# Performance work log

Measured on AMD Instinct MI355X. Metric: run time of the kernel, lower is better.

The kernel has to match this reference:

```python
import jax, jax.numpy as jnp
import numpy as np
import math

# Config (matches init_kwargs / input_specs)
N_ENT = 50000      # number of entities
N_REL = 500        # number of relations
HID = 64           # args.hidden_dim = per-axis dim d; entity dim = 3d, relation dim = 4d
E = 500000         # number of edges
EMB_RANGE = 1.0    # embedding_range
PI = 3.1415926235897933


def setup_inputs() -> dict:
    key = jax.random.key(0)
    k1, k2, k3, k4, k5 = jax.random.split(key, 5)
    entities = jax.random.normal(k1, (N_ENT, 3 * HID), dtype=jnp.float32)
    relations = jax.random.normal(k2, (N_REL, 4 * HID), dtype=jnp.float32)
    head = jax.random.randint(k3, (E,), 0, N_ENT, dtype=jnp.int32)
    rel = jax.random.randint(k4, (E,), 0, N_REL, dtype=jnp.int32)
    tail = jax.random.randint(k5, (E,), 0, N_ENT, dtype=jnp.int32)
    edge_index = jnp.stack([head, rel, tail], axis=0)  # (3, E)
    return {"entities": entities, "relations": relations, "edge_index": edge_index}


def do_trans(ent, rel):
    """Rot3DE rotation: rotate 3D entity point (per feature dim) by the
    quaternion encoded in rel = (axis_x, axis_y, axis_z, theta). is_head_rel=True branch.
    ent: (E, 3d), rel: (E, 4d) -> (E, 4d)"""
    ex, ey, ez = jnp.split(ent, 3, axis=-1)            # each (E, d)
    rx, ry, rz, theta = jnp.split(rel, 4, axis=-1)     # each (E, d)
    theta = theta / (EMB_RANGE / PI)
    sin = jnp.sin(theta)
    w = jnp.cos(theta)
    # F.normalize(stack([sin*rx, sin*ry, sin*rz]), dim=0): unit rotation axis (sign of sin folded in)
    t = jnp.stack([sin * rx, sin * ry, sin * rz], axis=0)  # (3, E, d)
    norm = jnp.sqrt(jnp.sum(t * t, axis=0, keepdims=True))
    n = t / jnp.maximum(norm, 1e-12)
    # quaternion q = (w, u) with u = |sin(theta)| * unit_axis  (sin sign already in n)
    s = jnp.sqrt(jnp.clip(1.0 - w * w, 0.0, None))
    ux, uy, uz = s * n[0], s * n[1], s * n[2]
    # Hamilton product q (x) p with pure quaternion p = (0, ex, ey, ez)  [head direction]
    x_score = w * ex + (uy * ez - uz * ey)
    y_score = w * ey + (uz * ex - ux * ez)
    z_score = w * ez + (ux * ey - uy * ex)
    w_score = -(ux * ex + uy * ey + uz * ez)
    return jnp.concatenate([x_score, y_score, z_score, w_score], axis=-1)  # (E, 4d)


def reference(entities, relations, edge_index):
    head, rel_id, tail = edge_index[0], edge_index[1], edge_index[2]
    # eff_do_trans's unique-based dedup is a pure compute optimization; the
    # math is identical to the direct per-edge transform below.
    qv = do_trans(entities[head], relations[rel_id])  # (E, 4d) keys/values
    # GAT_update: key = [gathered tail entity (3d) ; zeros(d)]
    k = jnp.concatenate(
        [entities[tail], jnp.zeros((E, HID), dtype=entities.dtype)], axis=-1
    )  # (E, 4d)
    embed_dim = 4 * HID
    alpha = jnp.sum(k * qv, axis=-1) / math.sqrt(embed_dim)  # (E,)
    # scatter_softmax over destination nodes (stable segment softmax)
    m = jax.ops.segment_max(alpha, tail, num_segments=N_ENT)
    m = jnp.where(jnp.isfinite(m), m, 0.0)  # empty segments
    e = jnp.exp(alpha - m[tail])
    denom = jax.ops.segment_sum(e, tail, num_segments=N_ENT)
    attn = e / denom[tail]  # (E,)
    # weighted scatter_add -> (N_ENT, 4d)
    out = jax.ops.segment_sum(qv * attn[:, None], tail, num_segments=N_ENT)
    return out
```

## Files before the change

### kernel.cpp

```cpp
#include <hip/hip_runtime.h>
#include <stdint.h>
#include <math.h>

#define HID 64
#define PI_F 3.14159262235897933f

__device__ __forceinline__ unsigned short f2bf(float f) {
    unsigned u = __float_as_uint(f);
    return (unsigned short)((u + 0x7FFFu + ((u >> 16) & 1u)) >> 16);
}
__device__ __forceinline__ float bflo(unsigned v) { return __uint_as_float(v << 16); }
__device__ __forceinline__ float bfhi(unsigned v) { return __uint_as_float(v & 0xFFFF0000u); }

__global__ void prep(const float* __restrict__ rel, uint2* __restrict__ quat16, int nrel,
                     const int* __restrict__ eidx, int E, int* __restrict__ hist,
                     const float* __restrict__ ent, uint4* __restrict__ ent16, int nconv,
                     int qblocks, int eblocks) {
    const int b = blockIdx.x;
    if (b < qblocks) {
        int i = b * 256 + threadIdx.x;
        if (i >= nrel * HID) return;
        int r = i >> 6, j = i & 63;
        const float* base = rel + (size_t)r * 4 * HID;
        float rx = base[j];
        float ry = base[HID + j];
        float rz = base[2 * HID + j];
        float th = base[3 * HID + j];
        float theta = th * PI_F;
        float sn = sinf(theta);
        float w  = cosf(theta);
        float tx = sn * rx, ty = sn * ry, tz = sn * rz;
        float norm = sqrtf(tx * tx + ty * ty + tz * tz);
        float inv = 1.0f / fmaxf(norm, 1e-12f);
        float s = sqrtf(fmaxf(1.0f - w * w, 0.0f));
        float ux = s * tx * inv, uy = s * ty * inv, uz = s * tz * inv;
        quat16[i] = make_uint2(((unsigned)f2bf(ux) << 16) | f2bf(w),
                               ((unsigned)f2bf(uz) << 16) | f2bf(uy));
    } else if (b < qblocks + eblocks) {
        int e = (b - qblocks) * 256 + threadIdx.x;
        if (e >= E) return;
        atomicAdd(hist + eidx[2 * E + e], 1);
    } else {
        int u = (b - qblocks - eblocks) * 256 + threadIdx.x;
        if (u >= nconv) return;
        const float4* src = (const float4*)ent + 2 * (size_t)u;
        float4 a = src[0], c = src[1];
        ent16[u] = make_uint4(((unsigned)f2bf(a.y) << 16) | f2bf(a.x),
                              ((unsigned)f2bf(a.w) << 16) | f2bf(a.z),
                              ((unsigned)f2bf(c.y) << 16) | f2bf(c.x),
                              ((unsigned)f2bf(c.w) << 16) | f2bf(c.z));
    }
}

__global__ void scan1(const int* __restrict__ hist, int* __restrict__ base,
                      int* __restrict__ partial, int n) {
    __shared__ int buf[256];
    int tid = threadIdx.x;
    int gid = blockIdx.x * 256 + tid;
    int v = (gid < n) ? hist[gid] : 0;
    buf[tid] = v;
    __syncthreads();
    #pragma unroll
    for (int off = 1; off < 256; off <<= 1) {
        int x = (tid >= off) ? buf[tid - off] : 0;
        __syncthreads();
        buf[tid] += x;
        __syncthreads();
    }
    if (gid < n) base[gid] = buf[tid] - v;
    if (tid == 255) partial[blockIdx.x] = buf[255];
}

__global__ void scan23(int* __restrict__ base, int* __restrict__ base2,
                       const int* __restrict__ partial,
                       int nb, int n, int E) {
    __shared__ int buf[256];
    int tid = threadIdx.x;
    int v = (tid < nb) ? partial[tid] : 0;
    buf[tid] = v;
    __syncthreads();
    #pragma unroll
    for (int off = 1; off < 256; off <<= 1) {
        int x = (tid >= off) ? buf[tid - off] : 0;
        __syncthreads();
        buf[tid] += x;
        __syncthreads();
    }
    int bsum = ((int)blockIdx.x < nb) ? partial[blockIdx.x] : 0;
    int boff = buf[blockIdx.x] - bsum;
    int gid = blockIdx.x * 256 + tid;
    if (gid < n) {
        int bv = base[gid] + boff;
        base[gid] = bv;
        base2[gid] = bv;
    } else if (gid == n) {
        base[n] = E;
    }
}

__global__ void scatter_hr(const int* __restrict__ eidx, int E,
                           int* __restrict__ base2,
                           int2* __restrict__ hr) {
    int e = blockIdx.x * blockDim.x + threadIdx.x;
    if (e >= E) return;
    int t = eidx[2 * E + e];
    int pos = atomicAdd(base2 + t, 1);
    hr[pos] = make_int2(eidx[e], eidx[E + e]);
}

template <bool BF16>
__global__ void __launch_bounds__(256)
seg_reduce(const float* __restrict__ ent,
           const uint2* __restrict__ ent16,
           const uint2* __restrict__ quat16,
           const int2* __restrict__ hr,
           const int* __restrict__ base,
           int n_ent,
           float* __restrict__ out) {
    const int lane = threadIdx.x & 63;
    const int sub = lane >> 4;
    const int j   = lane & 15;
    const int wid = (blockIdx.x * blockDim.x + threadIdx.x) >> 6;
    const int nw  = (gridDim.x * blockDim.x) >> 6;

    for (int t = wid; t < n_ent; t += nw) {
        int start = base[t];
        int end   = base[t + 1];
        float4* o4 = (float4*)(out + (size_t)t * (4 * HID));
        if (start == end) {
            o4[lane] = make_float4(0.f, 0.f, 0.f, 0.f);
            continue;
        }
        int last = end - 1;

        const float4* krow = (const float4*)(ent + (size_t)t * (3 * HID));
        float4 kx = krow[j], ky = krow[16 + j], kz = krow[32 + j];

        float dnm = 0.0f;
        float4 ax = make_float4(0.f, 0.f, 0.f, 0.f);
        float4 ay = ax, az = ax, aw = ax;

        for (int k0 = start; k0 < end; k0 += 4) {
            int e = k0 + sub;
            bool valid = (e < end);
            int2 her = hr[min(e, last)];

            float4 hx, hy, hz;
            if constexpr (BF16) {
                const uint2* h = ent16 + (size_t)her.x * 48;
                uint2 u0 = h[j], u1 = h[16 + j], u2 = h[32 + j];
                hx = make_float4(bflo(u0.x), bfhi(u0.x), bflo(u0.y), bfhi(u0.y));
                hy = make_float4(bflo(u1.x), bfhi(u1.x), bflo(u1.y), bfhi(u1.y));
                hz = make_float4(bflo(u2.x), bfhi(u2.x), bflo(u2.y), bfhi(u2.y));
            } else {
                const float4* h = (const float4*)(ent + (size_t)her.x * (3 * HID));
                hx = h[j]; hy = h[16 + j]; hz = h[32 + j];
            }
            const uint4* qr = (const uint4*)(quat16 + (size_t)her.y * HID + 4 * j);
            uint4 qa = qr[0], qb = qr[1];
            float4 q0 = make_float4(bflo(qa.x), bfhi(qa.x), bflo(qa.y), bfhi(qa.y));
            float4 q1 = make_float4(bflo(qa.z), bfhi(qa.z), bflo(qa.w), bfhi(qa.w));
            float4 q2 = make_float4(bflo(qb.x), bfhi(qb.x), bflo(qb.y), bfhi(qb.y));
            float4 q3 = make_float4(bflo(qb.z), bfhi(qb.z), bflo(qb.w), bfhi(qb.w));

            float4 qx, qy, qz, qw;
            float p = 0.0f;
            #define DO_DIM(F, Q) { \
                float ex = hx.F, ey = hy.F, ez = hz.F; \
                float w = Q.x, ux = Q.y, uy = Q.z, uz = Q.w; \
                float rqx = w * ex + uy * ez - uz * ey; \
                float rqy = w * ey + uz * ex - ux * ez; \
                float rqz = w * ez + ux * ey - uy * ex; \
                float rqw = -(ux * ex + uy * ey + uz * ez); \
                p += kx.F * rqx + ky.F * rqy + kz.F * rqz; \
                qx.F = rqx; qy.F = rqy; qz.F = rqz; qw.F = rqw; }
            DO_DIM(x, q0)
            DO_DIM(y, q1)
            DO_DIM(z, q2)
            DO_DIM(w, q3)
            #undef DO_DIM

            p += __shfl_xor(p, 1, 64);
            p += __shfl_xor(p, 2, 64);
            p += __shfl_xor(p, 4, 64);
            p += __shfl_xor(p, 8, 64);

            float pe = valid ? __expf(p * 0.0625f) : 0.0f;
            dnm += pe;
            ax.x += pe * qx.x; ax.y += pe * qx.y; ax.z += pe * qx.z; ax.w += pe * qx.w;
            ay.x += pe * qy.x; ay.y += pe * qy.y; ay.z += pe * qy.z; ay.w += pe * qy.w;
            az.x += pe * qz.x; az.y += pe * qz.y; az.z += pe * qz.z; az.w += pe * qz.w;
            aw.x += pe * qw.x; aw.y += pe * qw.y; aw.z += pe * qw.z; aw.w += pe * qw.w;
        }

        #pragma unroll
        for (int mask = 16; mask <= 32; mask <<= 1) {
            dnm += __shfl_xor(dnm, mask, 64);
            ax.x += __shfl_xor(ax.x, mask, 64); ax.y += __shfl_xor(ax.y, mask, 64);
            ax.z += __shfl_xor(ax.z, mask, 64); ax.w += __shfl_xor(ax.w, mask, 64);
            ay.x += __shfl_xor(ay.x, mask, 64); ay.y += __shfl_xor(ay.y, mask, 64);
            ay.z += __shfl_xor(ay.z, mask, 64); ay.w += __shfl_xor(ay.w, mask, 64);
            az.x += __shfl_xor(az.x, mask, 64); az.y += __shfl_xor(az.y, mask, 64);
            az.z += __shfl_xor(az.z, mask, 64); az.w += __shfl_xor(az.w, mask, 64);
            aw.x += __shfl_xor(aw.x, mask, 64); aw.y += __shfl_xor(aw.y, mask, 64);
            aw.z += __shfl_xor(aw.z, mask, 64); aw.w += __shfl_xor(aw.w, mask, 64);
        }

        float inv = (dnm > 0.0f) ? 1.0f / dnm : 0.0f;
        float4 lo = (sub & 1) ? ay : ax;
        float4 hi = (sub & 1) ? aw : az;
        float4 val = (sub & 2) ? hi : lo;
        val.x *= inv; val.y *= inv; val.z *= inv; val.w *= inv;
        o4[lane] = val;
    }
}

extern "C" void kernel_launch(void* const* d_in, const int* in_sizes, int n_in,
                              void* d_out, int out_size, void* d_ws, size_t ws_size,
                              hipStream_t stream) {
    const float* ent  = (const float*)d_in[0];
    const float* rel  = (const float*)d_in[1];
    const int*   eidx = (const int*)d_in[2];
    float* out = (float*)d_out;

    const int n_ent = in_sizes[0] / (3 * HID);
    const int n_rel = in_sizes[1] / (4 * HID);
    const int E     = in_sizes[2] / 3;

    uint8_t* wp = (uint8_t*)d_ws;
    int2* hr     = (int2*)wp;                        wp += (size_t)E * sizeof(int2);
    int*  hist   = (int*)wp;                         wp += (size_t)n_ent * 4;
    int*  base   = (int*)wp;                         wp += (size_t)(n_ent + 1) * 4;
    int*  base2  = (int*)wp;                         wp += (size_t)n_ent * 4;
    int*  partial= (int*)wp;                         wp += 256 * 4;
    wp = (uint8_t*)(((uintptr_t)wp + 15) & ~(uintptr_t)15);
    uint2* quat16 = (uint2*)wp;                      wp += (size_t)n_rel * HID * sizeof(uint2);
    wp = (uint8_t*)(((uintptr_t)wp + 15) & ~(uintptr_t)15);
    uint4* ent16 = (uint4*)wp;                       wp += (size_t)n_ent * 3 * HID * 2;
    const bool use16 = ((size_t)(wp - (uint8_t*)d_ws) <= ws_size);

    hipMemsetAsync(hist, 0, (size_t)n_ent * sizeof(int), stream);

    const int qblocks = (n_rel * HID + 255) / 256;
    const int eblocks = (E + 255) / 256;
    const int nconv   = use16 ? (n_ent * 3 * HID / 8) : 0;
    const int cblocks = (nconv + 255) / 256;
    prep<<<qblocks + eblocks + cblocks, 256, 0, stream>>>(
        rel, quat16, n_rel, eidx, E, hist, ent, ent16, nconv, qblocks, eblocks);

    const int nb = (n_ent + 255) / 256;
    scan1<<<nb, 256, 0, stream>>>(hist, base, partial, n_ent);
    scan23<<<(n_ent + 1 + 255) / 256, 256, 0, stream>>>(base, base2, partial, nb, n_ent, E);

    scatter_hr<<<eblocks, 256, 0, stream>>>(eidx, E, base2, hr);

    if (use16) {
        seg_reduce<true><<<2048, 256, 0, stream>>>(ent, (const uint2*)ent16, quat16,
                                                   hr, base, n_ent, out);
    } else {
        seg_reduce<false><<<2048, 256, 0, stream>>>(ent, nullptr, quat16,
                                                    hr, base, n_ent, out);
    }
}
```

Measured before the change: 137.2 us.

## Process two edges per wavefront with 32-lane halves and packed float2 math

Reworks the segment-reduce kernel so each wavefront handles two edges per iteration, each on a 32-lane half owning two feature dimensions, instead of four edges on 16-lane quarters owning four dimensions. The scatter step now stores pre-scaled row offsets, which removes index multiplies in the hot loop, and the math uses 2-wide vector types that may map to packed FP32 instructions. This lowers per-lane register pressure and the number of cross-lane reductions after the loop. The cost is an extra shuffle step per edge and more iterations for high-degree nodes. The fp32 fallback path for when the bf16 entity copy does not fit in the workspace is removed, so the workspace size is no longer checked.

```diff
diff --git a/kernel.cpp b/kernel.cpp
--- a/kernel.cpp
+++ b/kernel.cpp
@@ -4,6 +4,8 @@
 
 #define HID 64
 #define PI_F 3.14159262235897933f
+
+typedef float v2f __attribute__((ext_vector_type(2)));
 
 __device__ __forceinline__ unsigned short f2bf(float f) {
     unsigned u = __float_as_uint(f);
@@ -105,113 +107,92 @@
     if (e >= E) return;
     int t = eidx[2 * E + e];
     int pos = atomicAdd(base2 + t, 1);
-    hr[pos] = make_int2(eidx[e], eidx[E + e]);
-}
-
-template <bool BF16>
+    hr[pos] = make_int2(eidx[e] * 96, eidx[E + e] * 32);
+}
+
 __global__ void __launch_bounds__(256)
 seg_reduce(const float* __restrict__ ent,
-           const uint2* __restrict__ ent16,
-           const uint2* __restrict__ quat16,
+           const unsigned* __restrict__ ent32,
+           const uint4* __restrict__ quat4,
            const int2* __restrict__ hr,
            const int* __restrict__ base,
            int n_ent,
            float* __restrict__ out) {
     const int lane = threadIdx.x & 63;
-    const int sub = lane >> 4;
-    const int j   = lane & 15;
+    const int half = lane >> 5;
+    const int j    = lane & 31;
     const int wid = (blockIdx.x * blockDim.x + threadIdx.x) >> 6;
     const int nw  = (gridDim.x * blockDim.x) >> 6;
 
     for (int t = wid; t < n_ent; t += nw) {
         int start = base[t];
         int end   = base[t + 1];
-        float4* o4 = (float4*)(out + (size_t)t * (4 * HID));
+        float2* o2 = (float2*)(out + (size_t)t * (4 * HID));
+        const int ob0 = half * 64 + j;
+        const int ob1 = ob0 + 32;
         if (start == end) {
-            o4[lane] = make_float4(0.f, 0.f, 0.f, 0.f);
+            o2[ob0] = make_float2(0.f, 0.f);
+            o2[ob1] = make_float2(0.f, 0.f);
             continue;
         }
         int last = end - 1;
 
-        const float4* krow = (const float4*)(ent + (size_t)t * (3 * HID));
-        float4 kx = krow[j], ky = krow[16 + j], kz = krow[32 + j];
+        const v2f* k2 = (const v2f*)(ent + (size_t)t * (3 * HID));
+        v2f kx = k2[j], ky = k2[32 + j], kz = k2[64 + j];
 
         float dnm = 0.0f;
-        float4 ax = make_float4(0.f, 0.f, 0.f, 0.f);
-        float4 ay = ax, az = ax, aw = ax;
-
-        for (int k0 = start; k0 < end; k0 += 4) {
-            int e = k0 + sub;
+        v2f fx = {0.f, 0.f}, fy = fx, fz = fx, fw = fx;
+
+        for (int kk = start; kk < end; kk += 2) {
+            int e = kk + half;
             bool valid = (e < end);
             int2 her = hr[min(e, last)];
 
-            float4 hx, hy, hz;
-            if constexpr (BF16) {
-                const uint2* h = ent16 + (size_t)her.x * 48;
-                uint2 u0 = h[j], u1 = h[16 + j], u2 = h[32 + j];
-                hx = make_float4(bflo(u0.x), bfhi(u0.x), bflo(u0.y), bfhi(u0.y));
-                hy = make_float4(bflo(u1.x), bfhi(u1.x), bflo(u1.y), bfhi(u1.y));
-                hz = make_float4(bflo(u2.x), bfhi(u2.x), bflo(u2.y), bfhi(u2.y));
-            } else {
-                const float4* h = (const float4*)(ent + (size_t)her.x * (3 * HID));
-                hx = h[j]; hy = h[16 + j]; hz = h[32 + j];
-            }
-            const uint4* qr = (const uint4*)(quat16 + (size_t)her.y * HID + 4 * j);
-            uint4 qa = qr[0], qb = qr[1];
-            float4 q0 = make_float4(bflo(qa.x), bfhi(qa.x), bflo(qa.y), bfhi(qa.y));
-            float4 q1 = make_float4(bflo(qa.z), bfhi(qa.z), bflo(qa.w), bfhi(qa.w));
-            float4 q2 = make_float4(bflo(qb.x), bfhi(qb.x), bflo(qb.y), bfhi(qb.y));
-            float4 q3 = make_float4(bflo(qb.z), bfhi(qb.z), bflo(qb.w), bfhi(qb.w));
-
-            float4 qx, qy, qz, qw;
-            float p = 0.0f;
-            #define DO_DIM(F, Q) { \
-                float ex = hx.F, ey = hy.F, ez = hz.F; \
-                float w = Q.x, ux = Q.y, uy = Q.z, uz = Q.w; \
-                float rqx = w * ex + uy * ez - uz * ey; \
-                float rqy = w * ey + uz * ex - ux * ez; \
-                float rqz = w * ez + ux * ey - uy * ex; \
-                float rqw = -(ux * ex + uy * ey + uz * ez); \
-                p += kx.F * rqx + ky.F * rqy + kz.F * rqz; \
-                qx.F = rqx; qy.F = rqy; qz.F = rqz; qw.F = rqw; }
-            DO_DIM(x, q0)
-            DO_DIM(y, q1)
-            DO_DIM(z, q2)
-            DO_DIM(w, q3)
-            #undef DO_DIM
-
+            const unsigned* hb = ent32 + her.x;
+            unsigned u0 = hb[j], u1 = hb[32 + j], u2 = hb[64 + j];
+            uint4 qa = quat4[her.y + j];
+
+            v2f ex = {bflo(u0), bfhi(u0)};
+            v2f ey = {bflo(u1), bfhi(u1)};
+            v2f ez = {bflo(u2), bfhi(u2)};
+            v2f w  = {bflo(qa.x), bflo(qa.z)};
+            v2f ux = {bfhi(qa.x), bfhi(qa.z)};
+            v2f uy = {bflo(qa.y), bflo(qa.w)};
+            v2f uz = {bfhi(qa.y), bfhi(qa.w)};
+
+            v2f rqx = w * ex + uy * ez - uz * ey;
+            v2f rqy = w * ey + uz * ex - ux * ez;
+            v2f rqz = w * ez + ux * ey - uy * ex;
+            v2f rqw = -(ux * ex + uy * ey + uz * ez);
+
+            v2f p2 = kx * rqx + ky * rqy + kz * rqz;
+            float p = p2.x + p2.y;
             p += __shfl_xor(p, 1, 64);
             p += __shfl_xor(p, 2, 64);
             p += __shfl_xor(p, 4, 64);
             p += __shfl_xor(p, 8, 64);
+            p += __shfl_xor(p, 16, 64);
 
             float pe = valid ? __expf(p * 0.0625f) : 0.0f;
+            v2f pe2 = {pe, pe};
             dnm += pe;
-            ax.x += pe * qx.x; ax.y += pe * qx.y; ax.z += pe * qx.z; ax.w += pe * qx.w;
-            ay.x += pe * qy.x; ay.y += pe * qy.y; ay.z += pe * qy.z; ay.w += pe * qy.w;
-            az.x += pe * qz.x; az.y += pe * qz.y; az.z += pe * qz.z; az.w += pe * qz.w;
-            aw.x += pe * qw.x; aw.y += pe * qw.y; aw.z += pe * qw.z; aw.w += pe * qw.w;
+            fx += pe2 * rqx;
+            fy += pe2 * rqy;
+            fz += pe2 * rqz;
+            fw += pe2 * rqw;
         }
 
-        #pragma unroll
-        for (int mask = 16; mask <= 32; mask <<= 1) {
-            dnm += __shfl_xor(dnm, mask, 64);
-            ax.x += __shfl_xor(ax.x, mask, 64); ax.y += __shfl_xor(ax.y, mask, 64);
-            ax.z += __shfl_xor(ax.z, mask, 64); ax.w += __shfl_xor(ax.w, mask, 64);
-            ay.x += __shfl_xor(ay.x, mask, 64); ay.y += __shfl_xor(ay.y, mask, 64);
-            ay.z += __shfl_xor(ay.z, mask, 64); ay.w += __shfl_xor(ay.w, mask, 64);
-            az.x += __shfl_xor(az.x, mask, 64); az.y += __shfl_xor(az.y, mask, 64);
-            az.z += __shfl_xor(az.z, mask, 64); az.w += __shfl_xor(az.w, mask, 64);
-            aw.x += __shfl_xor(aw.x, mask, 64); aw.y += __shfl_xor(aw.y, mask, 64);
-            aw.z += __shfl_xor(aw.z, mask, 64); aw.w += __shfl_xor(aw.w, mask, 64);
-        }
+        dnm += __shfl_xor(dnm, 32, 64);
+        fx.x += __shfl_xor(fx.x, 32, 64); fx.y += __shfl_xor(fx.y, 32, 64);
+        fy.x += __shfl_xor(fy.x, 32, 64); fy.y += __shfl_xor(fy.y, 32, 64);
+        fz.x += __shfl_xor(fz.x, 32, 64); fz.y += __shfl_xor(fz.y, 32, 64);
+        fw.x += __shfl_xor(fw.x, 32, 64); fw.y += __shfl_xor(fw.y, 32, 64);
 
         float inv = (dnm > 0.0f) ? 1.0f / dnm : 0.0f;
-        float4 lo = (sub & 1) ? ay : ax;
-        float4 hi = (sub & 1) ? aw : az;
-        float4 val = (sub & 2) ? hi : lo;
-        val.x *= inv; val.y *= inv; val.z *= inv; val.w *= inv;
-        o4[lane] = val;
+        v2f s0 = half ? fz : fx;
+        v2f s1 = half ? fw : fy;
+        o2[ob0] = make_float2(s0.x * inv, s0.y * inv);
+        o2[ob1] = make_float2(s1.x * inv, s1.y * inv);
     }
 }
 
@@ -228,22 +209,22 @@
     const int E     = in_sizes[2] / 3;
 
     uint8_t* wp = (uint8_t*)d_ws;
-    int2* hr     = (int2*)wp;                        wp += (size_t)E * sizeof(int2);
-    int*  hist   = (int*)wp;                         wp += (size_t)n_ent * 4;
-    int*  base   = (int*)wp;                         wp += (size_t)(n_ent + 1) * 4;
-    int*  base2  = (int*)wp;                         wp += (size_t)n_ent * 4;
-    int*  partial= (int*)wp;                         wp += 256 * 4;
+    int2* hr      = (int2*)wp;                       wp += (size_t)E * sizeof(int2);
+    int*  hist    = (int*)wp;                        wp += (size_t)n_ent * 4;
+    int*  base    = (int*)wp;                        wp += (size_t)(n_ent + 1) * 4;
+    int*  base2   = (int*)wp;                        wp += (size_t)n_ent * 4;
+    int*  partial = (int*)wp;                        wp += 256 * 4;
     wp = (uint8_t*)(((uintptr_t)wp + 15) & ~(uintptr_t)15);
     uint2* quat16 = (uint2*)wp;                      wp += (size_t)n_rel * HID * sizeof(uint2);
     wp = (uint8_t*)(((uintptr_t)wp + 15) & ~(uintptr_t)15);
-    uint4* ent16 = (uint4*)wp;                       wp += (size_t)n_ent * 3 * HID * 2;
-    const bool use16 = ((size_t)(wp - (uint8_t*)d_ws) <= ws_size);
-
-    hipMemsetAsync(hist, 0, (size_t)n_ent * sizeof(int), stream);
+    uint4* ent16  = (uint4*)wp;                      wp += (size_t)n_ent * 3 * HID * 2;
+    (void)ws_size;
+
+    hipMemsetAsync(hist, 0, (size_t)n_ent * 4, stream);
 
     const int qblocks = (n_rel * HID + 255) / 256;
     const int eblocks = (E + 255) / 256;
-    const int nconv   = use16 ? (n_ent * 3 * HID / 8) : 0;
+    const int nconv   = n_ent * 3 * HID / 8;
     const int cblocks = (nconv + 255) / 256;
     prep<<<qblocks + eblocks + cblocks, 256, 0, stream>>>(
         rel, quat16, n_rel, eidx, E, hist, ent, ent16, nconv, qblocks, eblocks);
@@ -254,11 +235,6 @@
 
     scatter_hr<<<eblocks, 256, 0, stream>>>(eidx, E, base2, hr);
 
-    if (use16) {
-        seg_reduce<true><<<2048, 256, 0, stream>>>(ent, (const uint2*)ent16, quat16,
-                                                   hr, base, n_ent, out);
-    } else {
-        seg_reduce<false><<<2048, 256, 0, stream>>>(ent, nullptr, quat16,
-                                                    hr, base, n_ent, out);
-    }
-}
+    seg_reduce<<<2048, 256, 0, stream>>>(ent, (const unsigned*)ent16, (const uint4*)quat16,
+                                         hr, base, n_ent, out);
+}
```

Measured after the change: 126.8 us. 1.08x faster.
